# Kernel tuning notes

Hardware: AMD Instinct MI355X
Metric: run time of the kernel (lower is better)

## Reference

```python
import jax, jax.numpy as jnp
import numpy as np

N_NODES = 100000
N_EDGES = 1600000
VOCAB = 10000
HIDDEN = 64
LAYERS = 3
N_GRAPHS = 512
OUT_DIM = 1


def setup_inputs() -> dict:
    key = jax.random.key(0)
    ks = jax.random.split(key, 8)
    feats = jax.random.randint(ks[0], (N_NODES,), 0, VOCAB)
    src = jax.random.randint(ks[1], (N_EDGES,), 0, N_NODES)
    dst = jax.random.randint(ks[2], (N_EDGES,), 0, N_NODES)
    graph_ids = jnp.sort(jax.random.randint(ks[3], (N_NODES,), 0, N_GRAPHS))
    emb_table = jax.random.normal(ks[4], (VOCAB, HIDDEN), jnp.float32) * 0.02
    Ws = jax.random.normal(ks[5], (LAYERS, HIDDEN, HIDDEN), jnp.float32) * (HIDDEN ** -0.5)
    bs = jnp.zeros((LAYERS, HIDDEN), jnp.float32)
    W_reg = jax.random.normal(ks[6], (HIDDEN, OUT_DIM), jnp.float32) * (HIDDEN ** -0.5)
    return {"feats": feats, "src": src, "dst": dst, "graph_ids": graph_ids,
            "n_graphs": N_GRAPHS, "emb_table": emb_table, "Ws": Ws, "bs": bs,
            "W_reg": W_reg}


def reference(feats, src, dst, graph_ids, n_graphs, emb_table, Ws, bs, W_reg):
    N = feats.shape[0]
    ones = jnp.ones(src.shape[0], jnp.float32)
    # DGL GraphConv norm='both': src normalized by out-degree^-1/2, dst by in-degree^-1/2,
    # degrees clamped to min 1 (allow_zero_in_degree=True).
    out_deg = jnp.maximum(jax.ops.segment_sum(ones, src, num_segments=N), 1.0)
    in_deg = jnp.maximum(jax.ops.segment_sum(ones, dst, num_segments=N), 1.0)
    norm_src = (out_deg ** -0.5)[:, None]  # [N,1]
    norm_dst = (in_deg ** -0.5)[:, None]
    h = emb_table[feats]  # [N, hidden]
    for i in range(Ws.shape[0]):  # fixed small layer count
        m = h * norm_src
        agg = jax.ops.segment_sum(m[src], dst, num_segments=N)  # SpMM scatter-add
        h = agg * norm_dst @ Ws[i] + bs[i]
        # dropout p=0 -> identity
    pooled = jax.ops.segment_sum(h, graph_ids, num_segments=n_graphs)  # SumPooling
    return pooled @ W_reg
```

## Files before the change

### kernel.cpp

```cpp
#include <hip/hip_runtime.h>

#define HIDDEN 64
#define RANGE 512
#define RSHIFT 9
#define RB 256
#define NWR 512
#define ECMAX 3328
#define RCAP 12288

__global__ __launch_bounds__(256) void pre_kernel(const float* __restrict__ emb,
                                                  const float* __restrict__ Ws,
                                                  const float* __restrict__ bs,
                                                  const float* __restrict__ Wreg,
                                                  float* __restrict__ wt,
                                                  float* __restrict__ embu, int V,
                                                  const int* __restrict__ src,
                                                  const int* __restrict__ dst,
                                                  unsigned* __restrict__ pairs,
                                                  unsigned short* __restrict__ srcb,
                                                  int* __restrict__ cnts_in,
                                                  int* __restrict__ offs_in,
                                                  int* __restrict__ cnts_out,
                                                  int* __restrict__ offs_out,
                                                  float* __restrict__ out, int out_n,
                                                  int E, int EC, int R) {
    __shared__ float u3[HIDDEN], u2[HIDDEN], u1[HIDDEN];
    __shared__ int hin[RB], hout[RB];
    __shared__ int tmp[256];
    __shared__ unsigned plds[ECMAX];
    __shared__ unsigned short slds[ECMAX];
    int t = threadIdx.x;
    int b = blockIdx.x;
    const float* W0 = Ws;
    const float* W1 = Ws + HIDDEN * HIDDEN;
    const float* W2 = Ws + 2 * HIDDEN * HIDDEN;
    if (t < HIDDEN) { float s = 0.f; for (int j = 0; j < HIDDEN; j++) s += W2[t*HIDDEN+j] * Wreg[j]; u3[t] = s; }
    __syncthreads();
    if (t < HIDDEN) { float s = 0.f; for (int j = 0; j < HIDDEN; j++) s += W1[t*HIDDEN+j] * u3[j]; u2[t] = s; }
    __syncthreads();
    if (t < HIDDEN) { float s = 0.f; for (int j = 0; j < HIDDEN; j++) s += W0[t*HIDDEN+j] * u2[j]; u1[t] = s; }
    __syncthreads();
    if (b == 0) {
        if (t < HIDDEN) {
            float c1v = bs[t] * u2[t];
            float c2v = bs[HIDDEN + t] * u3[t];
            float c3v = bs[2*HIDDEN + t] * Wreg[t];
#pragma unroll
            for (int off = 32; off > 0; off >>= 1) {
                c1v += __shfl_down(c1v, off, 64);
                c2v += __shfl_down(c2v, off, 64);
                c3v += __shfl_down(c3v, off, 64);
            }
            if (t == 0) { wt[64] = c1v; wt[65] = c2v; wt[66] = c3v; }
        }
        for (int i = t; i < out_n; i += 256) out[i] = 0.0f;
    }
    int lane = t & 63, warp = t >> 6, vs = lane >> 4, ln = lane & 15;
    int EV = (V + 15) >> 4;
    for (int task = b; task < EV; task += gridDim.x) {
        int v = task * 16 + warp * 4 + vs;
        if (v < V) {
            const float* row = emb + (size_t)v * HIDDEN;
            float acc = row[ln]*u1[ln] + row[16+ln]*u1[16+ln]
                      + row[32+ln]*u1[32+ln] + row[48+ln]*u1[48+ln];
            acc += __shfl_xor(acc, 1, 64);
            acc += __shfl_xor(acc, 2, 64);
            acc += __shfl_xor(acc, 4, 64);
            acc += __shfl_xor(acc, 8, 64);
            if (ln == 0) embu[v] = acc;
        }
    }
    for (int i = t; i < RB; i += 256) { hin[i] = 0; hout[i] = 0; }
    __syncthreads();
    int es = b * EC, ee = min(E, es + EC);
    int cntE = ee - es;
    for (int e = es + t; e < ee; e += 256) {
        atomicAdd(&hin[dst[e] >> RSHIFT], 1);
        atomicAdd(&hout[src[e] >> RSHIFT], 1);
    }
    __syncthreads();
    int vin = hin[t], vout = hout[t];
    tmp[t] = vin;
    __syncthreads();
    for (int off = 1; off < 256; off <<= 1) {
        int u = (t >= off) ? tmp[t - off] : 0;
        __syncthreads();
        tmp[t] += u;
        __syncthreads();
    }
    int ein = tmp[t] - vin;
    tmp[t] = vout;
    __syncthreads();
    for (int off = 1; off < 256; off <<= 1) {
        int u = (t >= off) ? tmp[t - off] : 0;
        __syncthreads();
        tmp[t] += u;
        __syncthreads();
    }
    int eout = tmp[t] - vout;
    if (t < R) {
        cnts_in [(size_t)t * NWR + b] = vin;
        offs_in [(size_t)t * NWR + b] = ein;
        cnts_out[(size_t)t * NWR + b] = vout;
        offs_out[(size_t)t * NWR + b] = eout;
    }
    hin[t] = ein;
    hout[t] = eout;
    __syncthreads();
    for (int e = es + t; e < ee; e += 256) {
        int s = src[e], d = dst[e];
        int r = d >> RSHIFT;
        int lr = atomicAdd(&hin[r], 1);
        plds[lr] = ((unsigned)(d - (r << RSHIFT)) << 17) | (unsigned)s;
        int r2 = s >> RSHIFT;
        int lr2 = atomicAdd(&hout[r2], 1);
        slds[lr2] = (unsigned short)(s - (r2 << RSHIFT));
    }
    __syncthreads();
    unsigned* pg = pairs + (size_t)b * EC;
    unsigned short* sg = srcb + (size_t)b * EC;
    for (int i = t; i < cntE; i += 256) pg[i] = plds[i];
    for (int i = t; i < cntE; i += 256) sg[i] = slds[i];
}

__global__ __launch_bounds__(256) void build_kernel(const unsigned* __restrict__ pairs,
                                                    const unsigned short* __restrict__ srcb,
                                                    const int* __restrict__ cnts_in,
                                                    const int* __restrict__ offs_in,
                                                    const int* __restrict__ cnts_out,
                                                    const int* __restrict__ offs_out,
                                                    const int* __restrict__ feats,
                                                    const float* __restrict__ embu,
                                                    int* __restrict__ rbeg,
                                                    int* __restrict__ rend,
                                                    int* __restrict__ col,
                                                    float* __restrict__ ndst,
                                                    float* __restrict__ nsrc,
                                                    float* __restrict__ y0,
                                                    int N, int EC) {
    __shared__ int cnt[RANGE];
    __shared__ int sc[RANGE];
    __shared__ int oh[RANGE];
    __shared__ int tmp[256];
    __shared__ int ccin[NWR], coin[NWR], ccout[NWR], coout[NWR];
    int r = blockIdx.x, t = threadIdx.x;
    int n0 = r << RSHIFT;
    int nn = min(RANGE, N - n0);
    for (int i = t; i < RANGE; i += 256) { cnt[i] = 0; oh[i] = 0; }
    for (int i = t; i < NWR; i += 256) {
        ccin[i]  = cnts_in [(size_t)r * NWR + i];
        coin[i]  = offs_in [(size_t)r * NWR + i];
        ccout[i] = cnts_out[(size_t)r * NWR + i];
        coout[i] = offs_out[(size_t)r * NWR + i];
    }
    __syncthreads();
    for (int b = t; b < NWR; b += 256) {
        const unsigned* run = pairs + (size_t)b * EC + coin[b];
        int c = ccin[b];
        for (int k = 0; k < c; k++) atomicAdd(&cnt[run[k] >> 17], 1);
    }
    for (int b = t; b < NWR; b += 256) {
        const unsigned short* run = srcb + (size_t)b * EC + coout[b];
        int c = ccout[b];
        for (int k = 0; k < c; k++) atomicAdd(&oh[run[k]], 1);
    }
    __syncthreads();
    int a0 = cnt[2 * t], a1 = cnt[2 * t + 1];
    tmp[t] = a0 + a1;
    __syncthreads();
    for (int off = 1; off < 256; off <<= 1) {
        int u = (t >= off) ? tmp[t - off] : 0;
        __syncthreads();
        tmp[t] += u;
        __syncthreads();
    }
    int c_in = tmp[255];
    int pre = (t > 0) ? tmp[t - 1] : 0;
    sc[2 * t] = pre;
    sc[2 * t + 1] = pre + a0;
    __syncthreads();
    int base = r * RCAP;
    for (int i = t; i < nn; i += 256) {
        int n = n0 + i;
        rbeg[n] = base + sc[i];
        rend[n] = base + sc[i] + cnt[i];
        ndst[n] = rsqrtf(fmaxf((float)cnt[i], 1.0f));
        float ns = rsqrtf(fmaxf((float)oh[i], 1.0f));
        nsrc[n] = ns;
        y0[n] = embu[feats[n]] * ns;
    }
    if (t < 32) col[base + c_in + t] = 0;
    __syncthreads();
    for (int b = t; b < NWR; b += 256) {
        const unsigned* run = pairs + (size_t)b * EC + coin[b];
        int c = ccin[b];
        for (int k = 0; k < c; k++) {
            unsigned w = run[k];
            int slot = atomicAdd(&sc[w >> 17], 1);
            col[base + slot] = (int)(w & 0x1ffff);
        }
    }
}

__global__ __launch_bounds__(256) void sspmm_kernel(const int* __restrict__ rbeg,
                                                    const int* __restrict__ rend,
                                                    const int* __restrict__ col,
                                                    const float* __restrict__ y,
                                                    const float* __restrict__ ndst,
                                                    const float* __restrict__ nsrc,
                                                    const float* __restrict__ wt, int cidx,
                                                    float* __restrict__ out,
                                                    int N, int NH, int scale_out) {
    int lane = threadIdx.x & 63;
    int warp = threadIdx.x >> 6;
    int ns_ = lane >> 4, ln = lane & 15;
    int nA = blockIdx.x * 16 + warp * 4 + ns_;
    int nB = nA + NH;
    int begA = 0, endA = 0, begB = 0, endB = 0;
    if (nA < NH) { begA = rbeg[nA]; endA = rend[nA]; }
    if (nB < N)  { begB = rbeg[nB]; endB = rend[nB]; }
    float accA = 0.0f, accB = 0.0f;
    int jA = begA + ln, jB = begB + ln;
#pragma unroll
    for (int it = 0; it < 2; it++) {
        int ja = jA + (it << 4), jb = jB + (it << 4);
        float va = y[col[ja]];
        float vb = y[col[jb]];
        accA += (ja < endA) ? va : 0.0f;
        accB += (jb < endB) ? vb : 0.0f;
    }
    for (int j = jA + 32; j < endA; j += 16) accA += y[col[j]];
    for (int j = jB + 32; j < endB; j += 16) accB += y[col[j]];
#pragma unroll
    for (int m = 1; m <= 8; m <<= 1) {
        accA += __shfl_xor(accA, m, 64);
        accB += __shfl_xor(accB, m, 64);
    }
    if (ln == 0) {
        float c = wt[cidx];
        if (nA < NH) {
            float o = accA * ndst[nA] + c;
            out[nA] = scale_out ? o * nsrc[nA] : o;
        }
        if (nB < N) {
            float o = accB * ndst[nB] + c;
            out[nB] = scale_out ? o * nsrc[nB] : o;
        }
    }
}

__global__ __launch_bounds__(256) void final_kernel(const int* __restrict__ gids,
                                                    const float* __restrict__ nodeval,
                                                    float* __restrict__ out, int N) {
    int n = blockIdx.x * 256 + threadIdx.x;
    int lane = threadIdx.x & 63;
    float v = 0.0f;
    int g = -1;
    if (n < N) { v = nodeval[n]; g = gids[n]; }
#pragma unroll
    for (int off = 1; off < 64; off <<= 1) {
        float u = __shfl_up(v, off, 64);
        int gu = __shfl_up(g, off, 64);
        if (lane >= off && gu == g) v += u;
    }
    int gn = __shfl_down(g, 1, 64);
    bool last = (lane == 63) || (gn != g);
    if (n < N && last) atomicAdd(&out[g], v);
}

extern "C" void kernel_launch(void* const* d_in, const int* in_sizes, int n_in,
                              void* d_out, int out_size, void* d_ws, size_t ws_size,
                              hipStream_t stream) {
    const int*   feats = (const int*)d_in[0];
    const int*   src   = (const int*)d_in[1];
    const int*   dst   = (const int*)d_in[2];
    const int*   gids  = (const int*)d_in[3];
    const float* emb   = (const float*)d_in[5];
    const float* Ws    = (const float*)d_in[6];
    const float* bs    = (const float*)d_in[7];
    const float* Wreg  = (const float*)d_in[8];
    float* out = (float*)d_out;

    int N = in_sizes[0];
    int E = in_sizes[1];
    int V = in_sizes[5] / HIDDEN;
    int NB = (N + 255) / 256;
    int R = (N + RANGE - 1) / RANGE;
    int EC = (E + NWR - 1) / NWR;
    int NH = (N + 1) / 2;
    int GS = (NH + 15) / 16;

    char* p = (char*)d_ws;
    int*   rbeg    = (int*)p;    p += (size_t)N * 4;
    int*   rend    = (int*)p;    p += (size_t)N * 4;
    float* nsrc    = (float*)p;  p += (size_t)N * 4;
    float* ndst    = (float*)p;  p += (size_t)N * 4;
    float* wt      = (float*)p;  p += 128 * 4;
    float* embu    = (float*)p;  p += (size_t)V * 4;
    float* y0      = (float*)p;  p += (size_t)N * 4;
    float* y1      = (float*)p;  p += (size_t)N * 4;
    float* y2      = (float*)p;  p += (size_t)N * 4;
    float* nodeval = (float*)p;  p += (size_t)N * 4;
    int*   cnts_in  = (int*)p;   p += (size_t)R * NWR * 4;
    int*   offs_in  = (int*)p;   p += (size_t)R * NWR * 4;
    int*   cnts_out = (int*)p;   p += (size_t)R * NWR * 4;
    int*   offs_out = (int*)p;   p += (size_t)R * NWR * 4;
    int*   col     = (int*)p;    p += (size_t)R * RCAP * 4;
    p = (char*)(((uintptr_t)p + 255) & ~(uintptr_t)255);
    unsigned* pairs = (unsigned*)p;            p += (size_t)NWR * EC * 4;
    unsigned short* srcb = (unsigned short*)p; p += (size_t)NWR * EC * 2;

    pre_kernel<<<NWR, 256, 0, stream>>>(emb, Ws, bs, Wreg, wt, embu, V,
                                        src, dst, pairs, srcb,
                                        cnts_in, offs_in, cnts_out, offs_out,
                                        out, out_size, E, EC, R);
    build_kernel<<<R, 256, 0, stream>>>(pairs, srcb, cnts_in, offs_in, cnts_out, offs_out,
                                        feats, embu, rbeg, rend, col, ndst, nsrc, y0, N, EC);

    sspmm_kernel<<<GS, 256, 0, stream>>>(rbeg, rend, col, y0, ndst, nsrc, wt, 64, y1, N, NH, 1);
    sspmm_kernel<<<GS, 256, 0, stream>>>(rbeg, rend, col, y1, ndst, nsrc, wt, 65, y2, N, NH, 1);
    sspmm_kernel<<<GS, 256, 0, stream>>>(rbeg, rend, col, y2, ndst, nsrc, wt, 66, nodeval, N, NH, 0);
    final_kernel<<<NB, 256, 0, stream>>>(gids, nodeval, out, N);
}
```

Baseline: 165.9 us.

## Fuse final pooling into last SpMM, double edge partitions, pack counts/offsets

Doubles the number of edge-partition blocks in the preprocessing kernel and loads each thread's edges into registers once, reusing them for both histogram and scatter passes. Per-partition counts and offsets are packed into a single 32-bit word, halving the metadata tables. The last SpMM is fused with graph sum pooling through a shared-memory bin per block followed by global atomics, which removes the final kernel launch and the nodeval round trip. The cost is more partitions for build_kernel to walk, more global atomics from each block's pooling bins, and a fixed 16-bit limit on the packed offsets and counts.

```diff
diff --git a/kernel.cpp b/kernel.cpp
--- a/kernel.cpp
+++ b/kernel.cpp
@@ -4,9 +4,11 @@
 #define RANGE 512
 #define RSHIFT 9
 #define RB 256
-#define NWR 512
-#define ECMAX 3328
+#define NWR 1024
+#define EPT 7
+#define ECMAX (EPT * 256)
 #define RCAP 12288
+#define OUTMAX 512
 
 __global__ __launch_bounds__(256) void pre_kernel(const float* __restrict__ emb,
                                                   const float* __restrict__ Ws,
@@ -18,10 +20,8 @@
                                                   const int* __restrict__ dst,
                                                   unsigned* __restrict__ pairs,
                                                   unsigned short* __restrict__ srcb,
-                                                  int* __restrict__ cnts_in,
-                                                  int* __restrict__ offs_in,
-                                                  int* __restrict__ cnts_out,
-                                                  int* __restrict__ offs_out,
+                                                  unsigned* __restrict__ tin,
+                                                  unsigned* __restrict__ tout,
                                                   float* __restrict__ out, int out_n,
                                                   int E, int EC, int R) {
     __shared__ float u3[HIDDEN], u2[HIDDEN], u1[HIDDEN];
@@ -70,13 +70,24 @@
             if (ln == 0) embu[v] = acc;
         }
     }
-    for (int i = t; i < RB; i += 256) { hin[i] = 0; hout[i] = 0; }
-    __syncthreads();
     int es = b * EC, ee = min(E, es + EC);
     int cntE = ee - es;
-    for (int e = es + t; e < ee; e += 256) {
-        atomicAdd(&hin[dst[e] >> RSHIFT], 1);
-        atomicAdd(&hout[src[e] >> RSHIFT], 1);
+    int se[EPT], de[EPT];
+#pragma unroll
+    for (int k = 0; k < EPT; k++) {
+        int e = es + t + (k << 8);
+        bool vld = e < ee;
+        se[k] = vld ? src[e] : -1;
+        de[k] = vld ? dst[e] : -1;
+    }
+    hin[t] = 0; hout[t] = 0;
+    __syncthreads();
+#pragma unroll
+    for (int k = 0; k < EPT; k++) {
+        if (de[k] >= 0) {
+            atomicAdd(&hin[de[k] >> RSHIFT], 1);
+            atomicAdd(&hout[se[k] >> RSHIFT], 1);
+        }
     }
     __syncthreads();
     int vin = hin[t], vout = hout[t];
@@ -99,22 +110,24 @@
     }
     int eout = tmp[t] - vout;
     if (t < R) {
-        cnts_in [(size_t)t * NWR + b] = vin;
-        offs_in [(size_t)t * NWR + b] = ein;
-        cnts_out[(size_t)t * NWR + b] = vout;
-        offs_out[(size_t)t * NWR + b] = eout;
+        tin [(size_t)t * NWR + b] = (unsigned)ein  | ((unsigned)vin  << 16);
+        tout[(size_t)t * NWR + b] = (unsigned)eout | ((unsigned)vout << 16);
     }
     hin[t] = ein;
     hout[t] = eout;
     __syncthreads();
-    for (int e = es + t; e < ee; e += 256) {
-        int s = src[e], d = dst[e];
-        int r = d >> RSHIFT;
-        int lr = atomicAdd(&hin[r], 1);
-        plds[lr] = ((unsigned)(d - (r << RSHIFT)) << 17) | (unsigned)s;
-        int r2 = s >> RSHIFT;
-        int lr2 = atomicAdd(&hout[r2], 1);
-        slds[lr2] = (unsigned short)(s - (r2 << RSHIFT));
+#pragma unroll
+    for (int k = 0; k < EPT; k++) {
+        if (de[k] >= 0) {
+            int r = de[k] >> RSHIFT;
+            int lr = atomicAdd(&hin[r], 1);
+            if (lr < ECMAX)
+                plds[lr] = ((unsigned)(de[k] - (r << RSHIFT)) << 17) | (unsigned)se[k];
+            int r2 = se[k] >> RSHIFT;
+            int lr2 = atomicAdd(&hout[r2], 1);
+            if (lr2 < ECMAX)
+                slds[lr2] = (unsigned short)(se[k] - (r2 << RSHIFT));
+        }
     }
     __syncthreads();
     unsigned* pg = pairs + (size_t)b * EC;
@@ -125,10 +138,8 @@
 
 __global__ __launch_bounds__(256) void build_kernel(const unsigned* __restrict__ pairs,
                                                     const unsigned short* __restrict__ srcb,
-                                                    const int* __restrict__ cnts_in,
-                                                    const int* __restrict__ offs_in,
-                                                    const int* __restrict__ cnts_out,
-                                                    const int* __restrict__ offs_out,
+                                                    const unsigned* __restrict__ tin,
+                                                    const unsigned* __restrict__ tout,
                                                     const int* __restrict__ feats,
                                                     const float* __restrict__ embu,
                                                     int* __restrict__ rbeg,
@@ -142,26 +153,26 @@
     __shared__ int sc[RANGE];
     __shared__ int oh[RANGE];
     __shared__ int tmp[256];
-    __shared__ int ccin[NWR], coin[NWR], ccout[NWR], coout[NWR];
+    __shared__ unsigned pin[NWR], pout[NWR];
     int r = blockIdx.x, t = threadIdx.x;
     int n0 = r << RSHIFT;
     int nn = min(RANGE, N - n0);
     for (int i = t; i < RANGE; i += 256) { cnt[i] = 0; oh[i] = 0; }
     for (int i = t; i < NWR; i += 256) {
-        ccin[i]  = cnts_in [(size_t)r * NWR + i];
-        coin[i]  = offs_in [(size_t)r * NWR + i];
-        ccout[i] = cnts_out[(size_t)r * NWR + i];
-        coout[i] = offs_out[(size_t)r * NWR + i];
+        pin[i]  = tin [(size_t)r * NWR + i];
+        pout[i] = tout[(size_t)r * NWR + i];
     }
     __syncthreads();
     for (int b = t; b < NWR; b += 256) {
-        const unsigned* run = pairs + (size_t)b * EC + coin[b];
-        int c = ccin[b];
+        unsigned w = pin[b];
+        const unsigned* run = pairs + (size_t)b * EC + (w & 0xffff);
+        int c = (int)(w >> 16);
         for (int k = 0; k < c; k++) atomicAdd(&cnt[run[k] >> 17], 1);
     }
     for (int b = t; b < NWR; b += 256) {
-        const unsigned short* run = srcb + (size_t)b * EC + coout[b];
-        int c = ccout[b];
+        unsigned w = pout[b];
+        const unsigned short* run = srcb + (size_t)b * EC + (w & 0xffff);
+        int c = (int)(w >> 16);
         for (int k = 0; k < c; k++) atomicAdd(&oh[run[k]], 1);
     }
     __syncthreads();
@@ -192,12 +203,13 @@
     if (t < 32) col[base + c_in + t] = 0;
     __syncthreads();
     for (int b = t; b < NWR; b += 256) {
-        const unsigned* run = pairs + (size_t)b * EC + coin[b];
-        int c = ccin[b];
+        unsigned w = pin[b];
+        const unsigned* run = pairs + (size_t)b * EC + (w & 0xffff);
+        int c = (int)(w >> 16);
         for (int k = 0; k < c; k++) {
-            unsigned w = run[k];
-            int slot = atomicAdd(&sc[w >> 17], 1);
-            col[base + slot] = (int)(w & 0x1ffff);
+            unsigned wv = run[k];
+            int slot = atomicAdd(&sc[wv >> 17], 1);
+            col[base + slot] = (int)(wv & 0x1ffff);
         }
     }
 }
@@ -210,7 +222,7 @@
                                                     const float* __restrict__ nsrc,
                                                     const float* __restrict__ wt, int cidx,
                                                     float* __restrict__ out,
-                                                    int N, int NH, int scale_out) {
+                                                    int N, int NH) {
     int lane = threadIdx.x & 63;
     int warp = threadIdx.x >> 6;
     int ns_ = lane >> 4, ln = lane & 15;
@@ -238,34 +250,59 @@
     }
     if (ln == 0) {
         float c = wt[cidx];
-        if (nA < NH) {
-            float o = accA * ndst[nA] + c;
-            out[nA] = scale_out ? o * nsrc[nA] : o;
-        }
-        if (nB < N) {
-            float o = accB * ndst[nB] + c;
-            out[nB] = scale_out ? o * nsrc[nB] : o;
-        }
-    }
-}
-
-__global__ __launch_bounds__(256) void final_kernel(const int* __restrict__ gids,
-                                                    const float* __restrict__ nodeval,
-                                                    float* __restrict__ out, int N) {
-    int n = blockIdx.x * 256 + threadIdx.x;
-    int lane = threadIdx.x & 63;
-    float v = 0.0f;
-    int g = -1;
-    if (n < N) { v = nodeval[n]; g = gids[n]; }
-#pragma unroll
-    for (int off = 1; off < 64; off <<= 1) {
-        float u = __shfl_up(v, off, 64);
-        int gu = __shfl_up(g, off, 64);
-        if (lane >= off && gu == g) v += u;
-    }
-    int gn = __shfl_down(g, 1, 64);
-    bool last = (lane == 63) || (gn != g);
-    if (n < N && last) atomicAdd(&out[g], v);
+        if (nA < NH) out[nA] = (accA * ndst[nA] + c) * nsrc[nA];
+        if (nB < N)  out[nB] = (accB * ndst[nB] + c) * nsrc[nB];
+    }
+}
+
+__global__ __launch_bounds__(256) void sspmmf_kernel(const int* __restrict__ rbeg,
+                                                     const int* __restrict__ rend,
+                                                     const int* __restrict__ col,
+                                                     const float* __restrict__ y,
+                                                     const float* __restrict__ ndst,
+                                                     const float* __restrict__ wt,
+                                                     const int* __restrict__ gids,
+                                                     float* __restrict__ out,
+                                                     int N, int NH, int out_n) {
+    __shared__ float sbin[OUTMAX];
+    int t = threadIdx.x;
+    for (int i = t; i < out_n; i += 256) sbin[i] = 0.0f;
+    __syncthreads();
+    int lane = t & 63;
+    int warp = t >> 6;
+    int ns_ = lane >> 4, ln = lane & 15;
+    int nA = blockIdx.x * 16 + warp * 4 + ns_;
+    int nB = nA + NH;
+    int begA = 0, endA = 0, begB = 0, endB = 0;
+    if (nA < NH) { begA = rbeg[nA]; endA = rend[nA]; }
+    if (nB < N)  { begB = rbeg[nB]; endB = rend[nB]; }
+    float accA = 0.0f, accB = 0.0f;
+    int jA = begA + ln, jB = begB + ln;
+#pragma unroll
+    for (int it = 0; it < 2; it++) {
+        int ja = jA + (it << 4), jb = jB + (it << 4);
+        float va = y[col[ja]];
+        float vb = y[col[jb]];
+        accA += (ja < endA) ? va : 0.0f;
+        accB += (jb < endB) ? vb : 0.0f;
+    }
+    for (int j = jA + 32; j < endA; j += 16) accA += y[col[j]];
+    for (int j = jB + 32; j < endB; j += 16) accB += y[col[j]];
+#pragma unroll
+    for (int m = 1; m <= 8; m <<= 1) {
+        accA += __shfl_xor(accA, m, 64);
+        accB += __shfl_xor(accB, m, 64);
+    }
+    if (ln == 0) {
+        float c = wt[66];
+        if (nA < NH) atomicAdd(&sbin[gids[nA]], accA * ndst[nA] + c);
+        if (nB < N)  atomicAdd(&sbin[gids[nB]], accB * ndst[nB] + c);
+    }
+    __syncthreads();
+    for (int i = t; i < out_n; i += 256) {
+        float v = sbin[i];
+        if (v != 0.0f) atomicAdd(&out[i], v);
+    }
 }
 
 extern "C" void kernel_launch(void* const* d_in, const int* in_sizes, int n_in,
@@ -284,7 +321,6 @@
     int N = in_sizes[0];
     int E = in_sizes[1];
     int V = in_sizes[5] / HIDDEN;
-    int NB = (N + 255) / 256;
     int R = (N + RANGE - 1) / RANGE;
     int EC = (E + NWR - 1) / NWR;
     int NH = (N + 1) / 2;
@@ -300,25 +336,20 @@
     float* y0      = (float*)p;  p += (size_t)N * 4;
     float* y1      = (float*)p;  p += (size_t)N * 4;
     float* y2      = (float*)p;  p += (size_t)N * 4;
-    float* nodeval = (float*)p;  p += (size_t)N * 4;
-    int*   cnts_in  = (int*)p;   p += (size_t)R * NWR * 4;
-    int*   offs_in  = (int*)p;   p += (size_t)R * NWR * 4;
-    int*   cnts_out = (int*)p;   p += (size_t)R * NWR * 4;
-    int*   offs_out = (int*)p;   p += (size_t)R * NWR * 4;
+    unsigned* tin  = (unsigned*)p;  p += (size_t)R * NWR * 4;
+    unsigned* tout = (unsigned*)p;  p += (size_t)R * NWR * 4;
     int*   col     = (int*)p;    p += (size_t)R * RCAP * 4;
     p = (char*)(((uintptr_t)p + 255) & ~(uintptr_t)255);
     unsigned* pairs = (unsigned*)p;            p += (size_t)NWR * EC * 4;
     unsigned short* srcb = (unsigned short*)p; p += (size_t)NWR * EC * 2;
 
     pre_kernel<<<NWR, 256, 0, stream>>>(emb, Ws, bs, Wreg, wt, embu, V,
-                                        src, dst, pairs, srcb,
-                                        cnts_in, offs_in, cnts_out, offs_out,
+                                        src, dst, pairs, srcb, tin, tout,
                                         out, out_size, E, EC, R);
-    build_kernel<<<R, 256, 0, stream>>>(pairs, srcb, cnts_in, offs_in, cnts_out, offs_out,
+    build_kernel<<<R, 256, 0, stream>>>(pairs, srcb, tin, tout,
                                         feats, embu, rbeg, rend, col, ndst, nsrc, y0, N, EC);
 
-    sspmm_kernel<<<GS, 256, 0, stream>>>(rbeg, rend, col, y0, ndst, nsrc, wt, 64, y1, N, NH, 1);
-    sspmm_kernel<<<GS, 256, 0, stream>>>(rbeg, rend, col, y1, ndst, nsrc, wt, 65, y2, N, NH, 1);
-    sspmm_kernel<<<GS, 256, 0, stream>>>(rbeg, rend, col, y2, ndst, nsrc, wt, 66, nodeval, N, NH, 0);
-    final_kernel<<<NB, 256, 0, stream>>>(gids, nodeval, out, N);
-}
+    sspmm_kernel<<<GS, 256, 0, stream>>>(rbeg, rend, col, y0, ndst, nsrc, wt, 64, y1, N, NH);
+    sspmm_kernel<<<GS, 256, 0, stream>>>(rbeg, rend, col, y1, ndst, nsrc, wt, 65, y2, N, NH);
+    sspmmf_kernel<<<GS, 256, 0, stream>>>(rbeg, rend, col, y2, ndst, wt, gids, out, N, NH, out_size);
+}
```

Result: slower. 171.9 us (+3.6%).
